# Performance work log

Hardware: AMD Instinct MI355X
Metric: run time of the kernel (lower is better)

Reference implementation:

```python
import jax, jax.numpy as jnp
import numpy as np
from jax import lax

DIM = 192
HEADS = 4
HIDDEN = int(DIM * 2.66)  # 510
B, H, W = 2, 64, 64
EPS_LN = 1e-6
EPS_NORM = 1e-12


def conv1x1(x, w, b):
    # x: (b,c,h,w), w: (o,c), b: (o,)
    return jnp.einsum('bchw,oc->bohw', x, w) + b[None, :, None, None]


def dwconv3x3(x, w, b):
    # depthwise 3x3, SAME padding; w: (C,1,3,3)
    c = x.shape[1]
    y = lax.conv_general_dilated(x, w, window_strides=(1, 1), padding='SAME',
                                 feature_group_count=c,
                                 dimension_numbers=('NCHW', 'OIHW', 'NCHW'))
    return y + b[None, :, None, None]


def layernorm2d(x, w, b):
    mean = jnp.mean(x, axis=(2, 3), keepdims=True)
    var = jnp.mean((x - mean) ** 2, axis=(2, 3), keepdims=True)
    return (x - mean) / jnp.sqrt(var + EPS_LN) * w[None, :, None, None] + b[None, :, None, None]


def mdta(x, qkv_w, qkv_b, qkv_dw_w, qkv_dw_b, temperature, proj_w, proj_b):
    b, c, h, w = x.shape
    qkv = dwconv3x3(conv1x1(x, qkv_w, qkv_b), qkv_dw_w, qkv_dw_b)
    q, k, v = jnp.split(qkv, 3, axis=1)
    dh = c // HEADS
    q = q.reshape(b, HEADS, dh, h * w)
    k = k.reshape(b, HEADS, dh, h * w)
    v = v.reshape(b, HEADS, dh, h * w)
    # L2-normalize over per-head channel dim (axis=2), like F.normalize(dim=2)
    q = q / jnp.maximum(jnp.linalg.norm(q, axis=2, keepdims=True), EPS_NORM)
    k = k / jnp.maximum(jnp.linalg.norm(k, axis=2, keepdims=True), EPS_NORM)
    # spatial attention map: (b, heads, HW, HW)
    attn = jnp.einsum('bhcn,bhcm->bhnm', q, k) * temperature[None]  # temp (heads,1,1)
    attn = jax.nn.softmax(attn, axis=-1)
    out = jnp.einsum('bhnm,bhcm->bhcn', attn, v)  # (b,heads,dh,HW)
    out = out.reshape(b, c, h, w)
    return conv1x1(out, proj_w, proj_b)


def gdfn(x, pin_w, pin_b, dw_w, dw_b, pout_w, pout_b):
    y = dwconv3x3(conv1x1(x, pin_w, pin_b), dw_w, dw_b)
    y1, y2 = jnp.split(y, 2, axis=1)
    y = jax.nn.gelu(y1, approximate=False) * y2
    return conv1x1(y, pout_w, pout_b)


def setup_inputs() -> dict:
    key = jax.random.key(0)
    ks = jax.random.split(key, 8)
    s = 0.02
    return {
        'x': jax.random.normal(ks[0], (B, DIM, H, W), jnp.float32),
        'ln1_w': jnp.ones((DIM,), jnp.float32),
        'ln1_b': jnp.zeros((DIM,), jnp.float32),
        'qkv_w': jax.random.normal(ks[1], (DIM * 3, DIM), jnp.float32) * s,
        'qkv_b': jnp.zeros((DIM * 3,), jnp.float32),
        'qkv_dw_w': jax.random.normal(ks[2], (DIM * 3, 1, 3, 3), jnp.float32) * s,
        'qkv_dw_b': jnp.zeros((DIM * 3,), jnp.float32),
        'temperature': jnp.ones((HEADS, 1, 1), jnp.float32),
        'proj_w': jax.random.normal(ks[3], (DIM, DIM), jnp.float32) * s,
        'proj_b': jnp.zeros((DIM,), jnp.float32),
        'ln2_w': jnp.ones((DIM,), jnp.float32),
        'ln2_b': jnp.zeros((DIM,), jnp.float32),
        'pin_w': jax.random.normal(ks[4], (HIDDEN * 2, DIM), jnp.float32) * s,
        'pin_b': jnp.zeros((HIDDEN * 2,), jnp.float32),
        'gdfn_dw_w': jax.random.normal(ks[5], (HIDDEN * 2, 1, 3, 3), jnp.float32) * s,
        'gdfn_dw_b': jnp.zeros((HIDDEN * 2,), jnp.float32),
        'pout_w': jax.random.normal(ks[6], (DIM, HIDDEN), jnp.float32) * s,
        'pout_b': jnp.zeros((DIM,), jnp.float32),
    }


def reference(x, ln1_w, ln1_b, qkv_w, qkv_b, qkv_dw_w, qkv_dw_b, temperature,
              proj_w, proj_b, ln2_w, ln2_b, pin_w, pin_b, gdfn_dw_w, gdfn_dw_b,
              pout_w, pout_b):
    x = x + mdta(layernorm2d(x, ln1_w, ln1_b), qkv_w, qkv_b, qkv_dw_w, qkv_dw_b,
                 temperature, proj_w, proj_b)
    x = x + gdfn(layernorm2d(x, ln2_w, ln2_b), pin_w, pin_b, gdfn_dw_w, gdfn_dw_b,
                 pout_w, pout_b)
    return x
```

## Files before the change

kernel.cpp:

```cpp
#include <hip/hip_runtime.h>
#include <hip/hip_bf16.h>

typedef __bf16 bf16x8 __attribute__((ext_vector_type(8)));
typedef __bf16 bf16x4 __attribute__((ext_vector_type(4)));
typedef __bf16 bf16x2 __attribute__((ext_vector_type(2)));
typedef float f32x4 __attribute__((ext_vector_type(4)));

#define HW 4096
#define DIMC 192
#define DH 48
#define HIDC 510
#define LOG2E 1.44269504088896f

__device__ __forceinline__ float exp2_fast(float x) {
#if __has_builtin(__builtin_amdgcn_exp2f)
  return __builtin_amdgcn_exp2f(x);
#else
  float r;
  asm("v_exp_f32 %0, %1\n\ts_nop 1" : "=v"(r) : "v"(x));
  return r;
#endif
}

__device__ __forceinline__ float rcp_fast(float x) {
#if __has_builtin(__builtin_amdgcn_rcpf)
  return __builtin_amdgcn_rcpf(x);
#else
  float r;
  asm("v_rcp_f32 %0, %1\n\ts_nop 1" : "=v"(r) : "v"(x));
  return r;
#endif
}

__device__ __forceinline__ float gelu_fast(float x) {
  float z = fabsf(x) * 0.70710678118654752f;
  float t = rcp_fast(fmaf(0.3275911f, z, 1.f));
  float p = t * fmaf(t, fmaf(t, fmaf(t, fmaf(t, 1.061405429f, -1.453152027f), 1.421413741f), -0.284496736f), 0.254829592f);
  float e = exp2_fast(-z * z * 1.4426950408889634f);
  float erfa = 1.f - p * e;
  float erfx = copysignf(erfa, x);
  return 0.5f * x * (1.f + erfx);
}

__global__ __launch_bounds__(256) void wcvt_ln_kernel(const float* __restrict__ qkv_w, const float* __restrict__ proj_w,
                                                      const float* __restrict__ pin_w, const float* __restrict__ pout_w,
                                                      __bf16* __restrict__ wb_qkv, __bf16* __restrict__ wb_proj,
                                                      __bf16* __restrict__ wb_pin, __bf16* __restrict__ wb_pout,
                                                      const float* __restrict__ x, const float* __restrict__ lw,
                                                      const float* __restrict__ lb, float* __restrict__ sc,
                                                      float* __restrict__ sh, float* __restrict__ lnsum) {
  __shared__ float red[8];
  if (blockIdx.x < 1725) {
    if (blockIdx.x == 0) {
      for (int i = threadIdx.x; i < 768; i += 256) lnsum[i] = 0.f;
    }
    int idx = blockIdx.x * 256 + threadIdx.x;
    if (idx < 110592) {
      wb_qkv[idx] = (__bf16)qkv_w[idx];
    } else if (idx < 147456) {
      int i = idx - 110592;
      wb_proj[i] = (__bf16)proj_w[i];
    } else if (idx < 343296) {
      int i = idx - 147456;
      wb_pin[i] = (__bf16)pin_w[i];
    } else if (idx < 441600) {
      int i = idx - 343296;
      int o = i >> 9, c = i & 511;
      wb_pout[i] = (c < HIDC) ? (__bf16)pout_w[o * HIDC + c] : (__bf16)0.f;
    }
    return;
  }
  int bc = blockIdx.x - 1725;
  int c = bc % DIMC;
  const float* row = x + (size_t)bc * HW;
  float s = 0.f, s2 = 0.f;
  for (int i = threadIdx.x * 4; i < HW; i += 1024) {
    f32x4 v = *(const f32x4*)&row[i];
    s += (v.x + v.y) + (v.z + v.w);
    s2 = fmaf(v.x, v.x, s2); s2 = fmaf(v.y, v.y, s2);
    s2 = fmaf(v.z, v.z, s2); s2 = fmaf(v.w, v.w, s2);
  }
  for (int off = 32; off; off >>= 1) { s += __shfl_down(s, off, 64); s2 += __shfl_down(s2, off, 64); }
  int wid = threadIdx.x >> 6;
  if ((threadIdx.x & 63) == 0) { red[wid] = s; red[4 + wid] = s2; }
  __syncthreads();
  if (threadIdx.x == 0) {
    s = red[0] + red[1] + red[2] + red[3];
    s2 = red[4] + red[5] + red[6] + red[7];
    float mean = s * (1.f / HW);
    float var = s2 * (1.f / HW) - mean * mean;
    float rstd = rsqrtf(var + 1e-6f);
    float scv = rstd * lw[c];
    sc[bc] = scv;
    sh[bc] = lb[c] - mean * scv;
  }
}

__global__ __launch_bounds__(256) void ln_apply_t_kernel(const float* __restrict__ x, const float* __restrict__ sc,
                                                         const float* __restrict__ sh, __bf16* __restrict__ Xt) {
  int n0 = blockIdx.x * 64, c0 = blockIdx.y * 32, b = blockIdx.z;
  int t = threadIdx.x;
  int n = t & 63, cs = c0 + (t >> 6) * 8;
  __bf16 ob[8];
#pragma unroll
  for (int cc = 0; cc < 8; ++cc) {
    int c = cs + cc;
    float v = fmaf(x[((size_t)(b * DIMC + c)) * HW + n0 + n], sc[b * DIMC + c], sh[b * DIMC + c]);
    ob[cc] = (__bf16)v;
  }
  *(bf16x8*)&Xt[((size_t)((b << 12) + n0 + n)) * DIMC + cs] = *(bf16x8*)ob;
}

__global__ __launch_bounds__(256) void ln_apply_t_sum_kernel(const float* __restrict__ x, const float* __restrict__ lnsum,
                                                             const float* __restrict__ w, const float* __restrict__ bb,
                                                             __bf16* __restrict__ Xt) {
  int n0 = blockIdx.x * 64, c0 = blockIdx.y * 32, b = blockIdx.z;
  int t = threadIdx.x;
  int n = t & 63, cs = c0 + (t >> 6) * 8;
  __bf16 ob[8];
#pragma unroll
  for (int cc = 0; cc < 8; ++cc) {
    int c = cs + cc;
    float mean = lnsum[b * DIMC + c] * (1.f / HW);
    float var = lnsum[384 + b * DIMC + c] * (1.f / HW) - mean * mean;
    float rstd = rsqrtf(var + 1e-6f);
    float scv = rstd * w[c];
    float shv = bb[c] - mean * scv;
    float v = fmaf(x[((size_t)(b * DIMC + c)) * HW + n0 + n], scv, shv);
    ob[cc] = (__bf16)v;
  }
  *(bf16x8*)&Xt[((size_t)((b << 12) + n0 + n)) * DIMC + cs] = *(bf16x8*)ob;
}

__global__ __launch_bounds__(256) void gemm_kernel(const __bf16* __restrict__ A, const __bf16* __restrict__ Bt,
                                                   const float* __restrict__ bias, const float* __restrict__ res,
                                                   float* __restrict__ outf, __bf16* __restrict__ outb,
                                                   const float* __restrict__ part, float* __restrict__ lnsum,
                                                   int O, int Cs, int mode) {
  __shared__ __align__(16) __bf16 Asub[64 * 72];
  __shared__ __align__(16) __bf16 Bsub[128 * 72];
  __shared__ float linvS[4][128];
  const int t = threadIdx.x;
  const int lane = t & 63, wv = t >> 6;
  const int q4 = lane >> 4, l16 = lane & 15;
  int o0 = blockIdx.y * 64;
  if (o0 + 64 > O) o0 = O - 64;
  const int ntot0 = blockIdx.x * 128;
  const int b = ntot0 >> 12;
  const int n_in_b0 = ntot0 & 4095;

  if (mode == 4) {
#pragma unroll
    for (int jj = 0; jj < 2; ++jj) {
      int id = t + 256 * jj;
      int h = id >> 7, nl = id & 127;
      int n_in_b = n_in_b0 + nl;
      int ntb = n_in_b >> 6, n64 = n_in_b & 63;
      size_t pb = ((size_t)((b * 4 + h) * 64 + ntb)) * 3136 + 3072 + n64;
      float s = part[pb] + part[pb + (size_t)512 * 3136];
      linvS[h][nl] = rcp_fast(s);
    }
  }

  f32x4 acc[8];
#pragma unroll
  for (int nt = 0; nt < 8; ++nt) acc[nt] = (f32x4){0.f, 0.f, 0.f, 0.f};

  for (int c0 = 0; c0 < Cs; c0 += 64) {
    __syncthreads();
#pragma unroll
    for (int j = 0; j < 2; ++j) {
      int id = t + 256 * j;
      *(bf16x8*)&Asub[(id >> 3) * 72 + (id & 7) * 8] =
          *(const bf16x8*)&A[((size_t)(o0 + (id >> 3))) * Cs + c0 + (id & 7) * 8];
    }
    if (mode == 4) {
#pragma unroll
      for (int j = 0; j < 4; ++j) {
        int id = t + 256 * j;
        int row = id >> 3, cgrp = id & 7;
        int cglob = c0 + cgrp * 8;
        int h = cglob / 48;
        int cc = cglob - h * 48;
        int n_in_b = n_in_b0 + row;
        int ntb = n_in_b >> 6, n64 = n_in_b & 63;
        size_t pb = ((size_t)((b * 4 + h) * 64 + ntb)) * 3136 + (size_t)n64 * 48 + cc;
        f32x4 a0 = *(const f32x4*)&part[pb];
        f32x4 a1 = *(const f32x4*)&part[pb + 4];
        f32x4 b0 = *(const f32x4*)&part[pb + (size_t)512 * 3136];
        f32x4 b1 = *(const f32x4*)&part[pb + (size_t)512 * 3136 + 4];
        float li = linvS[h][row];
        f32x4 s0 = (a0 + b0) * li;
        f32x4 s1 = (a1 + b1) * li;
        bf16x8 ov = { (__bf16)s0.x, (__bf16)s0.y, (__bf16)s0.z, (__bf16)s0.w,
                      (__bf16)s1.x, (__bf16)s1.y, (__bf16)s1.z, (__bf16)s1.w };
        *(bf16x8*)&Bsub[row * 72 + cgrp * 8] = ov;
      }
    } else if (mode != 3) {
#pragma unroll
      for (int j = 0; j < 4; ++j) {
        int id = t + 256 * j;
        *(bf16x8*)&Bsub[(id >> 3) * 72 + (id & 7) * 8] =
            *(const bf16x8*)&Bt[((size_t)(ntot0 + (id >> 3))) * Cs + c0 + (id & 7) * 8];
      }
    } else {
      int cr = t & 63, seg = t >> 6;
      int cg = c0 + cr;
      __bf16 tmp[32];
      if (cg < HIDC) {
        const __bf16* gp = Bt + ((size_t)(b * HIDC + cg)) * HW + n_in_b0 + seg * 32;
#pragma unroll
        for (int j = 0; j < 4; ++j) *(bf16x8*)&tmp[8 * j] = *(const bf16x8*)&gp[8 * j];
      } else {
#pragma unroll
        for (int k = 0; k < 32; ++k) tmp[k] = (__bf16)0.f;
      }
#pragma unroll
      for (int k = 0; k < 32; ++k) Bsub[(seg * 32 + k) * 72 + cr] = tmp[k];
    }
    __syncthreads();
#pragma unroll
    for (int ks = 0; ks < 2; ++ks) {
      bf16x8 af = *(const bf16x8*)&Asub[(16 * wv + l16) * 72 + 32 * ks + 8 * q4];
#pragma unroll
      for (int nt = 0; nt < 8; ++nt) {
        bf16x8 bfr = *(const bf16x8*)&Bsub[(16 * nt + l16) * 72 + 32 * ks + 8 * q4];
        acc[nt] = __builtin_amdgcn_mfma_f32_16x16x32_bf16(af, bfr, acc[nt], 0, 0, 0);
      }
    }
  }

  float bvals[4];
#pragma unroll
  for (int r = 0; r < 4; ++r) bvals[r] = bias[o0 + 16 * wv + 4 * q4 + r];
  float osum[4] = {0.f, 0.f, 0.f, 0.f}, osq[4] = {0.f, 0.f, 0.f, 0.f};
#pragma unroll
  for (int nt = 0; nt < 8; ++nt) {
    int n_in_b = n_in_b0 + 16 * nt + l16;
#pragma unroll
    for (int r = 0; r < 4; ++r) {
      int o = o0 + 16 * wv + 4 * q4 + r;
      size_t addr = ((size_t)(b * O + o)) * HW + n_in_b;
      float v = acc[nt][r] + bvals[r];
      if (mode >= 2) { v += res[addr]; outf[addr] = v; }
      else if (mode == 0) { outf[addr] = v; }
      else { outb[addr] = (__bf16)v; }
      if (mode == 4) { osum[r] += v; osq[r] = fmaf(v, v, osq[r]); }
    }
  }
  if (mode == 4) {
#pragma unroll
    for (int r = 0; r < 4; ++r) {
      float s = osum[r], s2 = osq[r];
#pragma unroll
      for (int off = 1; off < 16; off <<= 1) {
        s += __shfl_xor(s, off, 64);
        s2 += __shfl_xor(s2, off, 64);
      }
      if (l16 == 0) {
        int o = o0 + 16 * wv + 4 * q4 + r;
        atomicAdd(&lnsum[b * DIMC + o], s);
        atomicAdd(&lnsum[384 + b * DIMC + o], s2);
      }
    }
  }
}

__global__ __launch_bounds__(256) void dwconv_split_kernel(const __bf16* __restrict__ in, const float* __restrict__ w,
                                                           const float* __restrict__ bias,
                                                           __bf16* __restrict__ qdwb, __bf16* __restrict__ Vbf) {
  int bc = blockIdx.x;
  int b = bc / 576, ch = bc - b * 576;
  __shared__ float tile[66 * 68];
  for (int i = threadIdx.x; i < 66 * 68; i += 256) tile[i] = 0.f;
  __syncthreads();
  const __bf16* p = in + (size_t)bc * HW;
  for (int j = 0; j < 8; ++j) {
    int i = 2 * threadIdx.x + 512 * j;
    bf16x2 v = *(const bf16x2*)&p[i];
    int y = i >> 6, xx = i & 63;
    tile[(y + 1) * 68 + xx + 1] = (float)v.x;
    tile[(y + 1) * 68 + xx + 2] = (float)v.y;
  }
  __syncthreads();
  float w0 = w[ch * 9 + 0], w1 = w[ch * 9 + 1], w2 = w[ch * 9 + 2];
  float w3 = w[ch * 9 + 3], w4 = w[ch * 9 + 4], w5 = w[ch * 9 + 5];
  float w6 = w[ch * 9 + 6], w7 = w[ch * 9 + 7], w8 = w[ch * 9 + 8];
  float bb = bias[ch];
  __bf16* dst;
  if (ch < 384) dst = qdwb + ((size_t)(b * 384 + ch)) * HW;
  else {
    int c = ch - 384, h = c / DH, cc = c - h * DH;
    dst = Vbf + ((size_t)((b * 4 + h) * DH + cc)) * HW;
  }
  for (int j = 0; j < 8; ++j) {
    int i = 2 * threadIdx.x + 512 * j;
    int y = i >> 6, xx = i & 63;
    const float* tt = &tile[y * 68 + xx];
    float a = bb;
    a = fmaf(w0, tt[0], a);   a = fmaf(w1, tt[1], a);   a = fmaf(w2, tt[2], a);
    a = fmaf(w3, tt[68], a);  a = fmaf(w4, tt[69], a);  a = fmaf(w5, tt[70], a);
    a = fmaf(w6, tt[136], a); a = fmaf(w7, tt[137], a); a = fmaf(w8, tt[138], a);
    float a2 = bb;
    a2 = fmaf(w0, tt[1], a2);   a2 = fmaf(w1, tt[2], a2);   a2 = fmaf(w2, tt[3], a2);
    a2 = fmaf(w3, tt[69], a2);  a2 = fmaf(w4, tt[70], a2);  a2 = fmaf(w5, tt[71], a2);
    a2 = fmaf(w6, tt[137], a2); a2 = fmaf(w7, tt[138], a2); a2 = fmaf(w8, tt[139], a2);
    bf16x2 o = { (__bf16)a, (__bf16)a2 };
    *(bf16x2*)&dst[i] = o;
  }
}

__global__ __launch_bounds__(256) void gdfn_dw_gate_kernel(const __bf16* __restrict__ hid, const float* __restrict__ w,
                                                           const float* __restrict__ bias, __bf16* __restrict__ gate) {
  int blk = blockIdx.x;
  int b = blk / HIDC, j = blk - b * HIDC;
  __shared__ __align__(16) float t1[66 * 68];
  __shared__ __align__(16) float t2[66 * 68];
  const int tid = threadIdx.x;
  if (tid < 136) {
    int r = (tid >= 68) ? 65 : 0;
    int c = (tid >= 68) ? tid - 68 : tid;
    t1[r * 68 + c] = 0.f;
    t2[r * 68 + c] = 0.f;
  }
  {
    int r = (tid >> 2) + 1;
    int c4 = tid & 3;
    int c = (c4 == 0) ? 0 : 64 + c4;
    t1[r * 68 + c] = 0.f;
    t2[r * 68 + c] = 0.f;
  }
  const __bf16* p1 = hid + ((size_t)b * (2 * HIDC) + j) * HW;
  const __bf16* p2 = p1 + (size_t)HIDC * HW;
  for (int jj = 0; jj < 8; ++jj) {
    int i = 2 * tid + 512 * jj;
    bf16x2 v1 = *(const bf16x2*)&p1[i];
    bf16x2 v2 = *(const bf16x2*)&p2[i];
    int y = i >> 6, xx = i & 63;
    t1[(y + 1) * 68 + xx + 1] = (float)v1.x;
    t1[(y + 1) * 68 + xx + 2] = (float)v1.y;
    t2[(y + 1) * 68 + xx + 1] = (float)v2.x;
    t2[(y + 1) * 68 + xx + 2] = (float)v2.y;
  }
  __syncthreads();
  int c1 = j, c2 = j + HIDC;
  float wa[9], wb[9];
#pragma unroll
  for (int k = 0; k < 9; ++k) { wa[k] = w[c1 * 9 + k]; wb[k] = w[c2 * 9 + k]; }
  float bi1 = bias[c1], bi2 = bias[c2];

  const int y = tid >> 2, x0 = 16 * (tid & 3);
  float x1v[16], x2v[16];
#pragma unroll
  for (int p = 0; p < 16; ++p) { x1v[p] = bi1; x2v[p] = bi2; }
#pragma unroll
  for (int r = 0; r < 3; ++r) {
    const float* rp1 = &t1[(y + r) * 68 + x0];
    float rr[20];
#pragma unroll
    for (int q = 0; q < 5; ++q) *(f32x4*)&rr[4 * q] = *(const f32x4*)&rp1[4 * q];
    float w0 = wa[3 * r], w1 = wa[3 * r + 1], w2 = wa[3 * r + 2];
#pragma unroll
    for (int p = 0; p < 16; ++p)
      x1v[p] = fmaf(w0, rr[p], fmaf(w1, rr[p + 1], fmaf(w2, rr[p + 2], x1v[p])));
  }
#pragma unroll
  for (int r = 0; r < 3; ++r) {
    const float* rp2 = &t2[(y + r) * 68 + x0];
    float rr[20];
#pragma unroll
    for (int q = 0; q < 5; ++q) *(f32x4*)&rr[4 * q] = *(const f32x4*)&rp2[4 * q];
    float w0 = wb[3 * r], w1 = wb[3 * r + 1], w2 = wb[3 * r + 2];
#pragma unroll
    for (int p = 0; p < 16; ++p)
      x2v[p] = fmaf(w0, rr[p], fmaf(w1, rr[p + 1], fmaf(w2, rr[p + 2], x2v[p])));
  }
  __bf16 ob[16];
#pragma unroll
  for (int p = 0; p < 16; ++p) ob[p] = (__bf16)(gelu_fast(x1v[p]) * x2v[p]);
  __bf16* op = gate + ((size_t)b * HIDC + j) * HW + y * 64 + x0;
  *(bf16x8*)&op[0] = *(bf16x8*)&ob[0];
  *(bf16x8*)&op[8] = *(bf16x8*)&ob[8];
}

__global__ __launch_bounds__(256) void prep_qk_kernel(const __bf16* __restrict__ qdwb, const float* __restrict__ temp,
                                                      __bf16* __restrict__ Qbf, __bf16* __restrict__ Kbf) {
  int t2 = blockIdx.x * 256 + threadIdx.x;
  int bh = t2 >> 11;
  int np = (t2 & 2047) * 2;
  int b = bh >> 2, h = bh & 3;
  const int isK = blockIdx.y;
  const __bf16* sp = qdwb + ((size_t)(b * 384 + isK * 192 + h * DH)) * HW + np;
  float tq = isK ? 1.f : temp[h] * LOG2E;

  bf16x2 raw[DH];
  float ss0 = 0.f, ss1 = 0.f;
#pragma unroll
  for (int c = 0; c < DH; ++c) {
    bf16x2 v = *(const bf16x2*)&sp[(size_t)c * HW];
    raw[c] = v;
    float f0 = (float)v.x, f1 = (float)v.y;
    ss0 = fmaf(f0, f0, ss0);
    ss1 = fmaf(f1, f1, ss1);
  }
  float sc0 = tq / fmaxf(sqrtf(ss0), 1e-12f);
  float sc1 = tq / fmaxf(sqrtf(ss1), 1e-12f);
  __bf16 ob0[64], ob1[64];
#pragma unroll
  for (int c = 0; c < DH; ++c) {
    ob0[c] = (__bf16)((float)raw[c].x * sc0);
    ob1[c] = (__bf16)((float)raw[c].y * sc1);
  }
#pragma unroll
  for (int c = DH; c < 64; ++c) { ob0[c] = (__bf16)0.f; ob1[c] = (__bf16)0.f; }
  __bf16* dd = (isK ? Kbf : Qbf) + ((size_t)(bh << 12) + np) * 64;
#pragma unroll
  for (int ch = 0; ch < 8; ++ch) {
    *(bf16x8*)&dd[ch * 8] = *(bf16x8*)&ob0[ch * 8];
    *(bf16x8*)&dd[64 + ch * 8] = *(bf16x8*)&ob1[ch * 8];
  }
}

__global__ __launch_bounds__(256) void attn_split_kernel(const __bf16* __restrict__ Qbf, const __bf16* __restrict__ Kbf,
                                                         const __bf16* __restrict__ Vbf, float* __restrict__ part) {
  __shared__ __align__(16) __bf16 Vc[2][48 * 72];
  __shared__ __align__(16) __bf16 Pl[2][64 * 72];
  const int tid = threadIdx.x;
  const int lane = tid & 63;
  const int wv = tid >> 6;
  const int q4 = lane >> 4, l16 = lane & 15;
  const int bid = blockIdx.x;
  const int chunk = bid >> 9, rest = bid & 511;
  const int bh = rest >> 6, nt = rest & 63;
  const int n0 = nt * 64;
  const __bf16* Qg = Qbf + (size_t)bh * HW * 64;
  const __bf16* Kg = Kbf + (size_t)bh * HW * 64;
  const __bf16* Vg = Vbf + (size_t)bh * DH * HW;

  bf16x8 qf[4][2];
#pragma unroll
  for (int s = 0; s < 4; ++s)
#pragma unroll
    for (int ks = 0; ks < 2; ++ks)
      qf[s][ks] = *(const bf16x8*)&Qg[((size_t)(n0 + 16 * s + l16)) * 64 + 32 * ks + 8 * q4];

  const int m0 = chunk * 2048;
  const __bf16* kp0 = Kg + ((size_t)(m0 + 16 * wv + l16)) * 64 + 8 * q4;
  const __bf16* kp1 = kp0 + 32;
  const __bf16* vp0 = Vg + ((size_t)(tid >> 3)) * HW + m0 + (tid & 7) * 8;
  const __bf16* vp1 = Vg + ((size_t)((tid + 256) >> 3)) * HW + m0 + ((tid + 256) & 7) * 8;
  bf16x8 kf0 = *(const bf16x8*)kp0;
  bf16x8 kf1 = *(const bf16x8*)kp1;
  bf16x8 vreg[2];
  vreg[0] = *(const bf16x8*)vp0;
  if (tid < 128) vreg[1] = *(const bf16x8*)vp1;

  float lsub[4] = {0.f, 0.f, 0.f, 0.f};
  f32x4 oacc[3];
#pragma unroll
  for (int ct = 0; ct < 3; ++ct) oacc[ct] = (f32x4){0.f, 0.f, 0.f, 0.f};

  for (int it = 0; it < 32; ++it) {
    const int cur = it & 1;
    *(bf16x8*)&Vc[cur][(tid >> 3) * 72 + (tid & 7) * 8] = vreg[0];
    if (tid < 128) {
      int i = tid + 256;
      *(bf16x8*)&Vc[cur][(i >> 3) * 72 + (i & 7) * 8] = vreg[1];
    }
    kp0 += 4096; kp1 += 4096; vp0 += 64; vp1 += 64;
    bf16x8 kn0 = *(const bf16x8*)kp0;
    bf16x8 kn1 = *(const bf16x8*)kp1;
    vreg[0] = *(const bf16x8*)vp0;
    if (tid < 128) vreg[1] = *(const bf16x8*)vp1;

    f32x4 sacc[4];
#pragma unroll
    for (int s = 0; s < 4; ++s) sacc[s] = (f32x4){0.f, 0.f, 0.f, 0.f};
    __builtin_amdgcn_s_setprio(1);
#pragma unroll
    for (int s = 0; s < 4; ++s)
      sacc[s] = __builtin_amdgcn_mfma_f32_16x16x32_bf16(kf0, qf[s][0], sacc[s], 0, 0, 0);
#pragma unroll
    for (int s = 0; s < 4; ++s)
      sacc[s] = __builtin_amdgcn_mfma_f32_16x16x32_bf16(kf1, qf[s][1], sacc[s], 0, 0, 0);
    __builtin_amdgcn_s_setprio(0);

#pragma unroll
    for (int s = 0; s < 4; ++s) {
      float p0 = exp2_fast(sacc[s][0]);
      float p1 = exp2_fast(sacc[s][1]);
      float p2 = exp2_fast(sacc[s][2]);
      float p3 = exp2_fast(sacc[s][3]);
      lsub[s] += (p0 + p1) + (p2 + p3);
      bf16x4 pk = { (__bf16)p0, (__bf16)p1, (__bf16)p2, (__bf16)p3 };
      *(bf16x4*)&Pl[cur][(16 * s + l16) * 72 + 16 * wv + 4 * q4] = pk;
    }
    __syncthreads();

    __builtin_amdgcn_s_setprio(1);
#pragma unroll
    for (int ks = 0; ks < 2; ++ks) {
      bf16x8 pf = *(const bf16x8*)&Pl[cur][(16 * wv + l16) * 72 + 32 * ks + 8 * q4];
#pragma unroll
      for (int ct = 0; ct < 3; ++ct) {
        bf16x8 vf = *(const bf16x8*)&Vc[cur][(16 * ct + l16) * 72 + 32 * ks + 8 * q4];
        oacc[ct] = __builtin_amdgcn_mfma_f32_16x16x32_bf16(pf, vf, oacc[ct], 0, 0, 0);
      }
    }
    __builtin_amdgcn_s_setprio(0);
    kf0 = kn0; kf1 = kn1;
  }

  __syncthreads();
  float* Lred = (float*)&Pl[0][0];
#pragma unroll
  for (int s = 0; s < 4; ++s) {
    float v = lsub[s];
    v += __shfl_xor(v, 16, 64);
    v += __shfl_xor(v, 32, 64);
    if (q4 == 0) Lred[wv * 64 + 16 * s + l16] = v;
  }
  __syncthreads();
  size_t pbase = (size_t)bid * 3136;
  if (tid < 64)
    part[pbase + 3072 + tid] = Lred[tid] + Lred[64 + tid] + Lred[128 + tid] + Lred[192 + tid];
#pragma unroll
  for (int ct = 0; ct < 3; ++ct)
#pragma unroll
    for (int r = 0; r < 4; ++r) {
      int n = 16 * wv + 4 * q4 + r;
      part[pbase + (size_t)n * 48 + 16 * ct + l16] = oacc[ct][r];
    }
}

extern "C" void kernel_launch(void* const* d_in, const int* in_sizes, int n_in,
                              void* d_out, int out_size, void* d_ws, size_t ws_size,
                              hipStream_t stream) {
  const float* x        = (const float*)d_in[0];
  const float* ln1_w    = (const float*)d_in[1];
  const float* ln1_b    = (const float*)d_in[2];
  const float* qkv_w    = (const float*)d_in[3];
  const float* qkv_b    = (const float*)d_in[4];
  const float* qkv_dw_w = (const float*)d_in[5];
  const float* qkv_dw_b = (const float*)d_in[6];
  const float* temperature = (const float*)d_in[7];
  const float* proj_w   = (const float*)d_in[8];
  const float* proj_b   = (const float*)d_in[9];
  const float* ln2_w    = (const float*)d_in[10];
  const float* ln2_b    = (const float*)d_in[11];
  const float* pin_w    = (const float*)d_in[12];
  const float* pin_b    = (const float*)d_in[13];
  const float* gdfn_dw_w = (const float*)d_in[14];
  const float* gdfn_dw_b = (const float*)d_in[15];
  const float* pout_w   = (const float*)d_in[16];
  const float* pout_b   = (const float*)d_in[17];
  float* out = (float*)d_out;
  float* ws = (float*)d_ws;

  __bf16* wb_qkv  = (__bf16*)(ws + 0);
  __bf16* wb_proj = (__bf16*)(ws + 55296);
  __bf16* wb_pin  = (__bf16*)(ws + 73728);
  __bf16* wb_pout = (__bf16*)(ws + 171648);
  float* sc1 = ws + 220800;
  float* sh1 = ws + 221184;
  float* lnsum = ws + 221568;
  __bf16* Xt1 = (__bf16*)(ws + 222336);
  __bf16* Xt2 = (__bf16*)(ws + 222336);
  __bf16* Qbf = (__bf16*)(ws + 222336);
  __bf16* Kbf = (__bf16*)(ws + 1270912);
  __bf16* Vbf = (__bf16*)(ws + 2319488);
  __bf16* qkvb   = (__bf16*)(ws + 3105920);
  __bf16* hid    = (__bf16*)(ws + 3105920);
  __bf16* qdwb  = (__bf16*)(ws + 5465216);
  float*  Opart = ws + 5465216;
  __bf16* gate  = (__bf16*)(ws + 7283840);

  wcvt_ln_kernel<<<1725 + 2 * DIMC, 256, 0, stream>>>(qkv_w, proj_w, pin_w, pout_w,
                                                      wb_qkv, wb_proj, wb_pin, wb_pout,
                                                      x, ln1_w, ln1_b, sc1, sh1, lnsum);
  ln_apply_t_kernel<<<dim3(64, 6, 2), 256, 0, stream>>>(x, sc1, sh1, Xt1);
  gemm_kernel<<<dim3(64, 9), 256, 0, stream>>>(wb_qkv, Xt1, qkv_b, nullptr, nullptr, qkvb,
                                               nullptr, nullptr, 576, 192, 1);
  dwconv_split_kernel<<<1152, 256, 0, stream>>>(qkvb, qkv_dw_w, qkv_dw_b, qdwb, Vbf);
  prep_qk_kernel<<<dim3(64, 2), 256, 0, stream>>>(qdwb, temperature, Qbf, Kbf);
  attn_split_kernel<<<1024, 256, 0, stream>>>(Qbf, Kbf, Vbf, Opart);
  gemm_kernel<<<dim3(64, 3), 256, 0, stream>>>(wb_proj, nullptr, proj_b, x, out, nullptr,
                                               Opart, lnsum, 192, 192, 4);

  ln_apply_t_sum_kernel<<<dim3(64, 6, 2), 256, 0, stream>>>(out, lnsum, ln2_w, ln2_b, Xt2);
  gemm_kernel<<<dim3(64, 16), 256, 0, stream>>>(wb_pin, Xt2, pin_b, nullptr, nullptr, hid,
                                                nullptr, nullptr, 1020, 192, 1);
  gdfn_dw_gate_kernel<<<2 * HIDC, 256, 0, stream>>>(hid, gdfn_dw_w, gdfn_dw_b, gate);
  gemm_kernel<<<dim3(64, 3), 256, 0, stream>>>(wb_pout, (const __bf16*)gate, pout_b, out, out, nullptr,
                                               nullptr, nullptr, 192, 512, 3);
}
```

Before: 233.8 us.

## Drop split-K attention partials; write normalized bf16 output directly for proj GEMM

Attention now processes the full key range per block instead of splitting it into two chunks. It normalizes by the softmax denominator in-kernel and writes bf16 output in the token-major layout the projection GEMM consumes. The GEMM's special combine mode is removed, and LN statistics accumulation is keyed on a non-null pointer. This removes a large fp32 partial write/read round trip, at the cost of half as many attention blocks, each doing twice the sequential work.

```diff
diff --git a/kernel.cpp b/kernel.cpp
--- a/kernel.cpp
+++ b/kernel.cpp
@@ -135,11 +135,10 @@
 __global__ __launch_bounds__(256) void gemm_kernel(const __bf16* __restrict__ A, const __bf16* __restrict__ Bt,
                                                    const float* __restrict__ bias, const float* __restrict__ res,
                                                    float* __restrict__ outf, __bf16* __restrict__ outb,
-                                                   const float* __restrict__ part, float* __restrict__ lnsum,
+                                                   float* __restrict__ lnsum,
                                                    int O, int Cs, int mode) {
   __shared__ __align__(16) __bf16 Asub[64 * 72];
   __shared__ __align__(16) __bf16 Bsub[128 * 72];
-  __shared__ float linvS[4][128];
   const int t = threadIdx.x;
   const int lane = t & 63, wv = t >> 6;
   const int q4 = lane >> 4, l16 = lane & 15;
@@ -149,19 +148,6 @@
   const int b = ntot0 >> 12;
   const int n_in_b0 = ntot0 & 4095;
 
-  if (mode == 4) {
-#pragma unroll
-    for (int jj = 0; jj < 2; ++jj) {
-      int id = t + 256 * jj;
-      int h = id >> 7, nl = id & 127;
-      int n_in_b = n_in_b0 + nl;
-      int ntb = n_in_b >> 6, n64 = n_in_b & 63;
-      size_t pb = ((size_t)((b * 4 + h) * 64 + ntb)) * 3136 + 3072 + n64;
-      float s = part[pb] + part[pb + (size_t)512 * 3136];
-      linvS[h][nl] = rcp_fast(s);
-    }
-  }
-
   f32x4 acc[8];
 #pragma unroll
   for (int nt = 0; nt < 8; ++nt) acc[nt] = (f32x4){0.f, 0.f, 0.f, 0.f};
@@ -174,29 +160,7 @@
       *(bf16x8*)&Asub[(id >> 3) * 72 + (id & 7) * 8] =
           *(const bf16x8*)&A[((size_t)(o0 + (id >> 3))) * Cs + c0 + (id & 7) * 8];
     }
-    if (mode == 4) {
-#pragma unroll
-      for (int j = 0; j < 4; ++j) {
-        int id = t + 256 * j;
-        int row = id >> 3, cgrp = id & 7;
-        int cglob = c0 + cgrp * 8;
-        int h = cglob / 48;
-        int cc = cglob - h * 48;
-        int n_in_b = n_in_b0 + row;
-        int ntb = n_in_b >> 6, n64 = n_in_b & 63;
-        size_t pb = ((size_t)((b * 4 + h) * 64 + ntb)) * 3136 + (size_t)n64 * 48 + cc;
-        f32x4 a0 = *(const f32x4*)&part[pb];
-        f32x4 a1 = *(const f32x4*)&part[pb + 4];
-        f32x4 b0 = *(const f32x4*)&part[pb + (size_t)512 * 3136];
-        f32x4 b1 = *(const f32x4*)&part[pb + (size_t)512 * 3136 + 4];
-        float li = linvS[h][row];
-        f32x4 s0 = (a0 + b0) * li;
-        f32x4 s1 = (a1 + b1) * li;
-        bf16x8 ov = { (__bf16)s0.x, (__bf16)s0.y, (__bf16)s0.z, (__bf16)s0.w,
-                      (__bf16)s1.x, (__bf16)s1.y, (__bf16)s1.z, (__bf16)s1.w };
-        *(bf16x8*)&Bsub[row * 72 + cgrp * 8] = ov;
-      }
-    } else if (mode != 3) {
+    if (mode != 3) {
 #pragma unroll
       for (int j = 0; j < 4; ++j) {
         int id = t + 256 * j;
@@ -245,10 +209,10 @@
       if (mode >= 2) { v += res[addr]; outf[addr] = v; }
       else if (mode == 0) { outf[addr] = v; }
       else { outb[addr] = (__bf16)v; }
-      if (mode == 4) { osum[r] += v; osq[r] = fmaf(v, v, osq[r]); }
-    }
-  }
-  if (mode == 4) {
+      if (lnsum) { osum[r] += v; osq[r] = fmaf(v, v, osq[r]); }
+    }
+  }
+  if (lnsum) {
 #pragma unroll
     for (int r = 0; r < 4; ++r) {
       float s = osum[r], s2 = osq[r];
@@ -422,7 +386,7 @@
 }
 
 __global__ __launch_bounds__(256) void attn_split_kernel(const __bf16* __restrict__ Qbf, const __bf16* __restrict__ Kbf,
-                                                         const __bf16* __restrict__ Vbf, float* __restrict__ part) {
+                                                         const __bf16* __restrict__ Vbf, __bf16* __restrict__ Xt) {
   __shared__ __align__(16) __bf16 Vc[2][48 * 72];
   __shared__ __align__(16) __bf16 Pl[2][64 * 72];
   const int tid = threadIdx.x;
@@ -430,8 +394,8 @@
   const int wv = tid >> 6;
   const int q4 = lane >> 4, l16 = lane & 15;
   const int bid = blockIdx.x;
-  const int chunk = bid >> 9, rest = bid & 511;
-  const int bh = rest >> 6, nt = rest & 63;
+  const int bh = bid >> 6, nt = bid & 63;
+  const int b = bh >> 2, h = bh & 3;
   const int n0 = nt * 64;
   const __bf16* Qg = Qbf + (size_t)bh * HW * 64;
   const __bf16* Kg = Kbf + (size_t)bh * HW * 64;
@@ -444,11 +408,10 @@
     for (int ks = 0; ks < 2; ++ks)
       qf[s][ks] = *(const bf16x8*)&Qg[((size_t)(n0 + 16 * s + l16)) * 64 + 32 * ks + 8 * q4];
 
-  const int m0 = chunk * 2048;
-  const __bf16* kp0 = Kg + ((size_t)(m0 + 16 * wv + l16)) * 64 + 8 * q4;
+  const __bf16* kp0 = Kg + ((size_t)(16 * wv + l16)) * 64 + 8 * q4;
   const __bf16* kp1 = kp0 + 32;
-  const __bf16* vp0 = Vg + ((size_t)(tid >> 3)) * HW + m0 + (tid & 7) * 8;
-  const __bf16* vp1 = Vg + ((size_t)((tid + 256) >> 3)) * HW + m0 + ((tid + 256) & 7) * 8;
+  const __bf16* vp0 = Vg + ((size_t)(tid >> 3)) * HW + (tid & 7) * 8;
+  const __bf16* vp1 = Vg + ((size_t)((tid + 256) >> 3)) * HW + ((tid + 256) & 7) * 8;
   bf16x8 kf0 = *(const bf16x8*)kp0;
   bf16x8 kf1 = *(const bf16x8*)kp1;
   bf16x8 vreg[2];
@@ -460,7 +423,7 @@
 #pragma unroll
   for (int ct = 0; ct < 3; ++ct) oacc[ct] = (f32x4){0.f, 0.f, 0.f, 0.f};
 
-  for (int it = 0; it < 32; ++it) {
+  for (int it = 0; it < 64; ++it) {
     const int cur = it & 1;
     *(bf16x8*)&Vc[cur][(tid >> 3) * 72 + (tid & 7) * 8] = vreg[0];
     if (tid < 128) {
@@ -521,15 +484,17 @@
     if (q4 == 0) Lred[wv * 64 + 16 * s + l16] = v;
   }
   __syncthreads();
-  size_t pbase = (size_t)bid * 3136;
+  float* Linv = Lred + 256;
   if (tid < 64)
-    part[pbase + 3072 + tid] = Lred[tid] + Lred[64 + tid] + Lred[128 + tid] + Lred[192 + tid];
+    Linv[tid] = rcp_fast(Lred[tid] + Lred[64 + tid] + Lred[128 + tid] + Lred[192 + tid]);
+  __syncthreads();
+  __bf16* od = Xt + ((size_t)((b << 12) + n0)) * DIMC + h * DH;
 #pragma unroll
   for (int ct = 0; ct < 3; ++ct)
 #pragma unroll
     for (int r = 0; r < 4; ++r) {
       int n = 16 * wv + 4 * q4 + r;
-      part[pbase + (size_t)n * 48 + 16 * ct + l16] = oacc[ct][r];
+      od[(size_t)n * DIMC + 16 * ct + l16] = (__bf16)(oacc[ct][r] * Linv[n]);
     }
 }
 
@@ -571,26 +536,26 @@
   __bf16* Vbf = (__bf16*)(ws + 2319488);
   __bf16* qkvb   = (__bf16*)(ws + 3105920);
   __bf16* hid    = (__bf16*)(ws + 3105920);
-  __bf16* qdwb  = (__bf16*)(ws + 5465216);
-  float*  Opart = ws + 5465216;
-  __bf16* gate  = (__bf16*)(ws + 7283840);
+  __bf16* qdwb   = (__bf16*)(ws + 5465216);
+  __bf16* Xt_att = (__bf16*)(ws + 5465216);
+  __bf16* gate   = (__bf16*)(ws + 7283840);
 
   wcvt_ln_kernel<<<1725 + 2 * DIMC, 256, 0, stream>>>(qkv_w, proj_w, pin_w, pout_w,
                                                       wb_qkv, wb_proj, wb_pin, wb_pout,
                                                       x, ln1_w, ln1_b, sc1, sh1, lnsum);
   ln_apply_t_kernel<<<dim3(64, 6, 2), 256, 0, stream>>>(x, sc1, sh1, Xt1);
   gemm_kernel<<<dim3(64, 9), 256, 0, stream>>>(wb_qkv, Xt1, qkv_b, nullptr, nullptr, qkvb,
-                                               nullptr, nullptr, 576, 192, 1);
+                                               nullptr, 576, 192, 1);
   dwconv_split_kernel<<<1152, 256, 0, stream>>>(qkvb, qkv_dw_w, qkv_dw_b, qdwb, Vbf);
   prep_qk_kernel<<<dim3(64, 2), 256, 0, stream>>>(qdwb, temperature, Qbf, Kbf);
-  attn_split_kernel<<<1024, 256, 0, stream>>>(Qbf, Kbf, Vbf, Opart);
-  gemm_kernel<<<dim3(64, 3), 256, 0, stream>>>(wb_proj, nullptr, proj_b, x, out, nullptr,
-                                               Opart, lnsum, 192, 192, 4);
+  attn_split_kernel<<<512, 256, 0, stream>>>(Qbf, Kbf, Vbf, Xt_att);
+  gemm_kernel<<<dim3(64, 3), 256, 0, stream>>>(wb_proj, Xt_att, proj_b, x, out, nullptr,
+                                               lnsum, 192, 192, 2);
 
   ln_apply_t_sum_kernel<<<dim3(64, 6, 2), 256, 0, stream>>>(out, lnsum, ln2_w, ln2_b, Xt2);
   gemm_kernel<<<dim3(64, 16), 256, 0, stream>>>(wb_pin, Xt2, pin_b, nullptr, nullptr, hid,
-                                                nullptr, nullptr, 1020, 192, 1);
+                                                nullptr, 1020, 192, 1);
   gdfn_dw_gate_kernel<<<2 * HIDC, 256, 0, stream>>>(hid, gdfn_dw_w, gdfn_dw_b, gate);
   gemm_kernel<<<dim3(64, 3), 256, 0, stream>>>(wb_pout, (const __bf16*)gate, pout_b, out, out, nullptr,
-                                               nullptr, nullptr, 192, 512, 3);
-}
+                                               nullptr, 192, 512, 3);
+}
```

After: 234.0 us (median of 2 runs). Within noise of the previous version (+0.1%).
